# Kernel optimization log

Measured on AMD Instinct MI355X. Metric: run time of the kernel, lower is better.

Reference implementation:

```python
import jax, jax.numpy as jnp
import numpy as np

B, IN, H = 8192, 1024, 1024

def setup_inputs() -> dict:
    key = jax.random.key(0)
    ks = jax.random.split(key, 12)
    s_i = 1.0 / np.sqrt(IN)   # lecun-normal-ish scale for input kernels
    s_h = 1.0 / np.sqrt(H)
    d = {
        'inputs': jax.random.normal(ks[0], (B, IN), jnp.float32),
        'c': jax.random.normal(ks[1], (B, H), jnp.float32),
        'h': jax.random.normal(ks[2], (B, H), jnp.float32),
    }
    for n, k in zip(['Wii', 'Wif', 'Wig', 'Wio'], ks[3:7]):
        d[n] = jax.random.normal(k, (IN, H), jnp.float32) * s_i
    for n, k in zip(['Whi', 'Whf', 'Whg', 'Who'], ks[7:11]):
        d[n] = jax.random.normal(k, (H, H), jnp.float32) * s_h
    for n in ['bi', 'bf', 'bg', 'bo']:
        d[n] = jnp.zeros((H,), jnp.float32)
    return d

def reference(inputs, c, h, Wii, Wif, Wig, Wio, Whi, Whf, Whg, Who, bi, bf, bg, bo):
    # i = sigmoid(x Wii + h Whi + bi); f, o likewise; g = tanh(x Wig + h Whg + bg)
    i = jax.nn.sigmoid(inputs @ Wii + h @ Whi + bi)
    f = jax.nn.sigmoid(inputs @ Wif + h @ Whf + bf)
    g = jnp.tanh(inputs @ Wig + h @ Whg + bg)
    o = jax.nn.sigmoid(inputs @ Wio + h @ Who + bo)
    new_c = f * c + i * g
    new_h = o * jnp.tanh(new_c)
    return (new_c, new_h)
```

## Files before the change

kernel.cpp:

```cpp
#include <hip/hip_runtime.h>
#include <hip/hip_bf16.h>
#include <cstdint>


#define B_DIM 8192
#define H_DIM 1024
#define K2    2048
#define N4    4096
#define BK    64

typedef __bf16 bf16x8 __attribute__((ext_vector_type(8)));
typedef __bf16 bf16x4 __attribute__((ext_vector_type(4)));
typedef float  f32x4  __attribute__((ext_vector_type(4)));

__device__ __forceinline__ void async_load16(const __bf16* g, __bf16* l) {
  __builtin_amdgcn_global_load_lds(
      (__attribute__((address_space(1))) void*)(g),
      (__attribute__((address_space(3))) void*)(l),
      16, 0, 0);
}

__device__ __forceinline__ float sigm(float x) {
  return 1.0f / (1.0f + __expf(-x));
}
__device__ __forceinline__ float tanh_fast(float x) {
  return 2.0f / (1.0f + __expf(-2.0f * x)) - 1.0f;
}

__global__ void cast_a(const float* __restrict__ x, const float* __restrict__ h,
                       __bf16* __restrict__ A) {
  int row = blockIdx.x;
  int k = threadIdx.x << 3;
  const float* src = (k < H_DIM) ? (x + (size_t)row * H_DIM + k)
                                 : (h + (size_t)row * H_DIM + (k - H_DIM));
  float4 v0 = *(const float4*)src;
  float4 v1 = *(const float4*)(src + 4);
  bf16x8 o;
  o[0] = (__bf16)v0.x; o[1] = (__bf16)v0.y; o[2] = (__bf16)v0.z; o[3] = (__bf16)v0.w;
  o[4] = (__bf16)v1.x; o[5] = (__bf16)v1.y; o[6] = (__bf16)v1.z; o[7] = (__bf16)v1.w;
  *(bf16x8*)&A[(size_t)row * K2 + k] = o;
}

__global__ void cast_w(const float* __restrict__ Wii, const float* __restrict__ Wif,
                       const float* __restrict__ Wig, const float* __restrict__ Wio,
                       const float* __restrict__ Whi, const float* __restrict__ Whf,
                       const float* __restrict__ Whg, const float* __restrict__ Who,
                       __bf16* __restrict__ Bt) {
  __shared__ float tile[32][33];
  int k0 = blockIdx.x * 32;
  int j0 = blockIdx.y * 32;
  int gate = blockIdx.z;
  const float* Wi[4] = {Wii, Wif, Wig, Wio};
  const float* Wh[4] = {Whi, Whf, Whg, Who};
  const float* W = (k0 < H_DIM) ? Wi[gate] : Wh[gate];
  int kb = (k0 < H_DIM) ? k0 : (k0 - H_DIM);

  int tx = threadIdx.x & 31;
  int ty = threadIdx.x >> 5;
  for (int kk = ty; kk < 32; kk += 8)
    tile[kk][tx] = W[(size_t)(kb + kk) * H_DIM + j0 + tx];
  __syncthreads();

  int jj = threadIdx.x >> 3;
  int kq = threadIdx.x & 7;
  int j = j0 + jj;
  int p = ((j >> 4) << 6) + (gate << 4) + (j & 15);
  bf16x4 o;
  o[0] = (__bf16)tile[kq * 4 + 0][jj];
  o[1] = (__bf16)tile[kq * 4 + 1][jj];
  o[2] = (__bf16)tile[kq * 4 + 2][jj];
  o[3] = (__bf16)tile[kq * 4 + 3][jj];
  *(bf16x4*)&Bt[(size_t)p * K2 + k0 + kq * 4] = o;
}

__global__ __launch_bounds__(256) void lstm_gemm(
    const __bf16* __restrict__ A,
    const __bf16* __restrict__ Bt,
    const float* __restrict__ c,
    const float* __restrict__ bi, const float* __restrict__ bf_,
    const float* __restrict__ bg, const float* __restrict__ bo,
    float* __restrict__ out_c, float* __restrict__ out_h) {
  __shared__ __align__(16) __bf16 As[128 * BK];
  __shared__ __align__(16) __bf16 Bs[128 * BK];

  const int tid  = threadIdx.x;
  const int wave = tid >> 6;
  const int lane = tid & 63;
  const int wm   = wave >> 1;
  const int wn   = wave & 1;
  const int m0   = blockIdx.x * 128;
  const int n0   = blockIdx.y * 128;

  f32x4 acc[4][4] = {};

  const int l15  = lane & 15;
  const int quad = lane >> 4;

  const int rin  = lane >> 3;
  const int slot = lane & 7;
  const int sg   = slot ^ rin;
  const __bf16* gA[4]; const __bf16* gB[4];
  __bf16* lA[4]; __bf16* lB[4];
#pragma unroll
  for (int c2 = 0; c2 < 4; ++c2) {
    int r = wave * 32 + c2 * 8 + rin;
    gA[c2] = A  + (size_t)(m0 + r) * K2 + sg * 8;
    gB[c2] = Bt + (size_t)(n0 + r) * K2 + sg * 8;
    lA[c2] = &As[(wave * 4 + c2) * 512];
    lB[c2] = &Bs[(wave * 4 + c2) * 512];
  }

  for (int k0 = 0; k0 < K2; k0 += BK) {
    __syncthreads();
#pragma unroll
    for (int c2 = 0; c2 < 4; ++c2) async_load16(gA[c2] + k0, lA[c2]);
#pragma unroll
    for (int c2 = 0; c2 < 4; ++c2) async_load16(gB[c2] + k0, lB[c2]);
    __syncthreads();

#pragma unroll
    for (int kk = 0; kk < 2; ++kk) {
      bf16x8 af[4], bfr[4];
      const int want = kk * 4 + quad;
      const int sw   = (want ^ (l15 & 7)) * 8;
#pragma unroll
      for (int t = 0; t < 4; ++t)
        af[t] = *(const bf16x8*)&As[(wm * 64 + t * 16 + l15) * BK + sw];
#pragma unroll
      for (int t = 0; t < 4; ++t)
        bfr[t] = *(const bf16x8*)&Bs[(wn * 64 + t * 16 + l15) * BK + sw];

#pragma unroll
      for (int tm = 0; tm < 4; ++tm)
#pragma unroll
        for (int tn = 0; tn < 4; ++tn)
          acc[tm][tn] = __builtin_amdgcn_mfma_f32_16x16x32_bf16(
              af[tm], bfr[tn], acc[tm][tn], 0, 0, 0);
    }
  }

  const int j = blockIdx.y * 32 + wn * 16 + l15;
  const float vbi = bi[j], vbf = bf_[j], vbg = bg[j], vbo = bo[j];

#pragma unroll
  for (int tm = 0; tm < 4; ++tm) {
#pragma unroll
    for (int r = 0; r < 4; ++r) {
      int row = m0 + wm * 64 + tm * 16 + quad * 4 + r;
      float gi = sigm(acc[tm][0][r] + vbi);
      float gf = sigm(acc[tm][1][r] + vbf);
      float gg = tanh_fast(acc[tm][2][r] + vbg);
      float go = sigm(acc[tm][3][r] + vbo);
      size_t idx = (size_t)row * H_DIM + j;
      float cv = c[idx];
      float nc = gf * cv + gi * gg;
      float nh = go * tanh_fast(nc);
      out_c[idx] = nc;
      out_h[idx] = nh;
    }
  }
}

extern "C" void kernel_launch(void* const* d_in, const int* in_sizes, int n_in,
                              void* d_out, int out_size, void* d_ws, size_t ws_size,
                              hipStream_t stream) {
  const float* x   = (const float*)d_in[0];
  const float* c   = (const float*)d_in[1];
  const float* h   = (const float*)d_in[2];
  const float* Wii = (const float*)d_in[3];
  const float* Wif = (const float*)d_in[4];
  const float* Wig = (const float*)d_in[5];
  const float* Wio = (const float*)d_in[6];
  const float* Whi = (const float*)d_in[7];
  const float* Whf = (const float*)d_in[8];
  const float* Whg = (const float*)d_in[9];
  const float* Who = (const float*)d_in[10];
  const float* bi  = (const float*)d_in[11];
  const float* bf_ = (const float*)d_in[12];
  const float* bg  = (const float*)d_in[13];
  const float* bo  = (const float*)d_in[14];

  __bf16* Abf = (__bf16*)d_ws;
  __bf16* Bt  = (__bf16*)((char*)d_ws + (size_t)B_DIM * K2 * 2);

  float* out_c = (float*)d_out;
  float* out_h = out_c + (size_t)B_DIM * H_DIM;

  cast_a<<<B_DIM, 256, 0, stream>>>(x, h, Abf);
  dim3 gw(K2 / 32, H_DIM / 32, 4);
  cast_w<<<gw, 256, 0, stream>>>(Wii, Wif, Wig, Wio, Whi, Whf, Whg, Who, Bt);
  dim3 gg(B_DIM / 128, N4 / 128);
  lstm_gemm<<<gg, 256, 0, stream>>>(Abf, Bt, c, bi, bf_, bg, bo, out_c, out_h);
}
```

Baseline: 367.2 us.

## Switch GEMM to 32x32x16 MFMA with 128x256 tiles and 32-wide gate interleave

The fused LSTM GEMM moves from 16x16x32 to 32x32x16 bf16 MFMA and widens the block tile from 128x128 to 128x256, so each wave computes 64x128. The weight packing changes to interleave gates in groups of 32 columns to match the new fragment layout, and cast_w now processes 64-deep k tiles with 8-element vector stores. The aim is more reuse per LDS read, fewer blocks loading A, and higher MFMA throughput. In exchange LDS use and register pressure rise (launch_bounds 256,2), and the grid has fewer blocks.

```diff
diff --git a/kernel.cpp b/kernel.cpp
--- a/kernel.cpp
+++ b/kernel.cpp
@@ -8,10 +8,13 @@
 #define K2    2048
 #define N4    4096
 #define BK    64
+#define BM    128
+#define BN    256
 
 typedef __bf16 bf16x8 __attribute__((ext_vector_type(8)));
 typedef __bf16 bf16x4 __attribute__((ext_vector_type(4)));
 typedef float  f32x4  __attribute__((ext_vector_type(4)));
+typedef float  f32x16 __attribute__((ext_vector_type(16)));
 
 __device__ __forceinline__ void async_load16(const __bf16* g, __bf16* l) {
   __builtin_amdgcn_global_load_lds(
@@ -46,8 +49,8 @@
                        const float* __restrict__ Whi, const float* __restrict__ Whf,
                        const float* __restrict__ Whg, const float* __restrict__ Who,
                        __bf16* __restrict__ Bt) {
-  __shared__ float tile[32][33];
-  int k0 = blockIdx.x * 32;
+  __shared__ float tile[64][33];
+  int k0 = blockIdx.x * 64;
   int j0 = blockIdx.y * 32;
   int gate = blockIdx.z;
   const float* Wi[4] = {Wii, Wif, Wig, Wio};
@@ -55,98 +58,100 @@
   const float* W = (k0 < H_DIM) ? Wi[gate] : Wh[gate];
   int kb = (k0 < H_DIM) ? k0 : (k0 - H_DIM);
 
-  int tx = threadIdx.x & 31;
-  int ty = threadIdx.x >> 5;
-  for (int kk = ty; kk < 32; kk += 8)
-    tile[kk][tx] = W[(size_t)(kb + kk) * H_DIM + j0 + tx];
+  int col = threadIdx.x & 31;
+  int rr  = threadIdx.x >> 5;
+#pragma unroll
+  for (int p = 0; p < 8; ++p)
+    tile[p * 8 + rr][col] = W[(size_t)(kb + p * 8 + rr) * H_DIM + j0 + col];
   __syncthreads();
 
   int jj = threadIdx.x >> 3;
-  int kq = threadIdx.x & 7;
+  int ko = threadIdx.x & 7;
   int j = j0 + jj;
-  int p = ((j >> 4) << 6) + (gate << 4) + (j & 15);
-  bf16x4 o;
-  o[0] = (__bf16)tile[kq * 4 + 0][jj];
-  o[1] = (__bf16)tile[kq * 4 + 1][jj];
-  o[2] = (__bf16)tile[kq * 4 + 2][jj];
-  o[3] = (__bf16)tile[kq * 4 + 3][jj];
-  *(bf16x4*)&Bt[(size_t)p * K2 + k0 + kq * 4] = o;
+  int p = ((j >> 5) << 7) + (gate << 5) + (j & 31);
+  bf16x8 o;
+#pragma unroll
+  for (int t = 0; t < 8; ++t) o[t] = (__bf16)tile[ko * 8 + t][jj];
+  *(bf16x8*)&Bt[(size_t)p * K2 + k0 + ko * 8] = o;
 }
 
-__global__ __launch_bounds__(256) void lstm_gemm(
+__global__ __launch_bounds__(256, 2) void lstm_gemm(
     const __bf16* __restrict__ A,
     const __bf16* __restrict__ Bt,
     const float* __restrict__ c,
     const float* __restrict__ bi, const float* __restrict__ bf_,
     const float* __restrict__ bg, const float* __restrict__ bo,
     float* __restrict__ out_c, float* __restrict__ out_h) {
-  __shared__ __align__(16) __bf16 As[128 * BK];
-  __shared__ __align__(16) __bf16 Bs[128 * BK];
+  __shared__ __align__(16) __bf16 As[BM * BK];
+  __shared__ __align__(16) __bf16 Bs[BN * BK];
 
   const int tid  = threadIdx.x;
   const int wave = tid >> 6;
   const int lane = tid & 63;
   const int wm   = wave >> 1;
   const int wn   = wave & 1;
-  const int m0   = blockIdx.x * 128;
-  const int n0   = blockIdx.y * 128;
+  const int m0   = blockIdx.x * BM;
+  const int n0   = blockIdx.y * BN;
 
-  f32x4 acc[4][4] = {};
+  f32x16 acc[2][4] = {};
 
-  const int l15  = lane & 15;
-  const int quad = lane >> 4;
+  const int l31 = lane & 31;
+  const int h8  = lane >> 5;
 
   const int rin  = lane >> 3;
   const int slot = lane & 7;
   const int sg   = slot ^ rin;
-  const __bf16* gA[4]; const __bf16* gB[4];
-  __bf16* lA[4]; __bf16* lB[4];
+  const __bf16* gA[4]; const __bf16* gB[8];
+  __bf16* lA[4]; __bf16* lB[8];
 #pragma unroll
-  for (int c2 = 0; c2 < 4; ++c2) {
-    int r = wave * 32 + c2 * 8 + rin;
-    gA[c2] = A  + (size_t)(m0 + r) * K2 + sg * 8;
-    gB[c2] = Bt + (size_t)(n0 + r) * K2 + sg * 8;
-    lA[c2] = &As[(wave * 4 + c2) * 512];
-    lB[c2] = &Bs[(wave * 4 + c2) * 512];
+  for (int cc = 0; cc < 4; ++cc) {
+    int r = wave * 32 + cc * 8 + rin;
+    gA[cc] = A + (size_t)(m0 + r) * K2 + sg * 8;
+    lA[cc] = &As[(wave * 4 + cc) * 512];
+  }
+#pragma unroll
+  for (int cc = 0; cc < 8; ++cc) {
+    int r = wave * 64 + cc * 8 + rin;
+    gB[cc] = Bt + (size_t)(n0 + r) * K2 + sg * 8;
+    lB[cc] = &Bs[(wave * 8 + cc) * 512];
   }
 
   for (int k0 = 0; k0 < K2; k0 += BK) {
     __syncthreads();
 #pragma unroll
-    for (int c2 = 0; c2 < 4; ++c2) async_load16(gA[c2] + k0, lA[c2]);
+    for (int cc = 0; cc < 4; ++cc) async_load16(gA[cc] + k0, lA[cc]);
 #pragma unroll
-    for (int c2 = 0; c2 < 4; ++c2) async_load16(gB[c2] + k0, lB[c2]);
+    for (int cc = 0; cc < 8; ++cc) async_load16(gB[cc] + k0, lB[cc]);
     __syncthreads();
 
 #pragma unroll
-    for (int kk = 0; kk < 2; ++kk) {
-      bf16x8 af[4], bfr[4];
-      const int want = kk * 4 + quad;
-      const int sw   = (want ^ (l15 & 7)) * 8;
+    for (int ks = 0; ks < 4; ++ks) {
+      bf16x8 af[2], bfr[4];
+      const int sw = ((ks * 2 + h8) ^ (l31 & 7)) * 8;
+#pragma unroll
+      for (int t = 0; t < 2; ++t)
+        af[t] = *(const bf16x8*)&As[(wm * 64 + t * 32 + l31) * BK + sw];
 #pragma unroll
       for (int t = 0; t < 4; ++t)
-        af[t] = *(const bf16x8*)&As[(wm * 64 + t * 16 + l15) * BK + sw];
-#pragma unroll
-      for (int t = 0; t < 4; ++t)
-        bfr[t] = *(const bf16x8*)&Bs[(wn * 64 + t * 16 + l15) * BK + sw];
+        bfr[t] = *(const bf16x8*)&Bs[(wn * 128 + t * 32 + l31) * BK + sw];
 
 #pragma unroll
-      for (int tm = 0; tm < 4; ++tm)
+      for (int tm = 0; tm < 2; ++tm)
 #pragma unroll
         for (int tn = 0; tn < 4; ++tn)
-          acc[tm][tn] = __builtin_amdgcn_mfma_f32_16x16x32_bf16(
+          acc[tm][tn] = __builtin_amdgcn_mfma_f32_32x32x16_bf16(
               af[tm], bfr[tn], acc[tm][tn], 0, 0, 0);
     }
   }
 
-  const int j = blockIdx.y * 32 + wn * 16 + l15;
+  const int j = blockIdx.y * 64 + wn * 32 + l31;
   const float vbi = bi[j], vbf = bf_[j], vbg = bg[j], vbo = bo[j];
 
 #pragma unroll
-  for (int tm = 0; tm < 4; ++tm) {
+  for (int tm = 0; tm < 2; ++tm) {
 #pragma unroll
-    for (int r = 0; r < 4; ++r) {
-      int row = m0 + wm * 64 + tm * 16 + quad * 4 + r;
+    for (int r = 0; r < 16; ++r) {
+      int row = m0 + wm * 64 + tm * 32 + 4 * h8 + (r & 3) + 8 * (r >> 2);
       float gi = sigm(acc[tm][0][r] + vbi);
       float gf = sigm(acc[tm][1][r] + vbf);
       float gg = tanh_fast(acc[tm][2][r] + vbg);
@@ -187,8 +192,8 @@
   float* out_h = out_c + (size_t)B_DIM * H_DIM;
 
   cast_a<<<B_DIM, 256, 0, stream>>>(x, h, Abf);
-  dim3 gw(K2 / 32, H_DIM / 32, 4);
+  dim3 gw(K2 / 64, H_DIM / 32, 4);
   cast_w<<<gw, 256, 0, stream>>>(Wii, Wif, Wig, Wio, Whi, Whf, Whg, Who, Bt);
-  dim3 gg(B_DIM / 128, N4 / 128);
+  dim3 gg(B_DIM / BM, N4 / BN);
   lstm_gemm<<<gg, 256, 0, stream>>>(Abf, Bt, c, bi, bf_, bg, bo, out_c, out_h);
 }
```

After: 347.7 us. 5.3% less time.
